# Optimization experiments

Measured on AMD Instinct MI355X. Metric: run time of the kernel, lower is better.

The kernel has to match this reference:

```python
import jax, jax.numpy as jnp
import numpy as np

B, S, E, H, D = 2, 4096, 512, 8, 64  # batch, seq, embed, heads, key_dim


def setup_inputs() -> dict:
    key = jax.random.key(0)
    ks = jax.random.split(key, 8)
    queries = jax.random.normal(ks[0], (B, S, E), dtype=jnp.float32)
    keys = jax.random.normal(ks[1], (B, S, E), dtype=jnp.float32)
    values = jax.random.normal(ks[2], (B, S, E), dtype=jnp.float32)
    mask = jax.random.randint(ks[3], (B, H, S, S), 0, 2).astype(bool)
    scale = 1.0 / np.sqrt(E)
    Wq = jax.random.normal(ks[4], (E, H * D), dtype=jnp.float32) * scale
    Wk = jax.random.normal(ks[5], (E, H * D), dtype=jnp.float32) * scale
    Wv = jax.random.normal(ks[6], (E, H * D), dtype=jnp.float32) * scale
    Wo = jax.random.normal(ks[7], (H * D, E), dtype=jnp.float32) * scale
    return {"queries": queries, "keys": keys, "values": values, "mask": mask,
            "Wq": Wq, "Wk": Wk, "Wv": Wv, "Wo": Wo}


def reference(queries, keys, values, mask, Wq, Wk, Wv, Wo):
    # QKV projections (no bias), reshape to heads: (B, S, H, D)
    q = (queries @ Wq).reshape(B, -1, H, D)
    k = (keys @ Wk).reshape(B, -1, H, D)
    v = (values @ Wv).reshape(B, -1, H, D)
    # scores: (B, H, Sq, Sk)
    scores = jnp.einsum("bqhd,bkhd->bhqk", q, k) / jnp.sqrt(jnp.float32(D))
    scores = jnp.where(mask, jnp.float32(-1e10), scores)
    attn = jax.nn.softmax(scores, axis=-1)
    out = jnp.einsum("bhqk,bkhd->bqhd", attn, v).reshape(B, -1, H * D)
    return out @ Wo
```

## Files before the change

kernel.cpp:

```cpp
#include <hip/hip_runtime.h>
#include <hip/hip_bf16.h>

#define NB 2
#define NS 4096
#define NE 512
#define NH 8
#define ND 64
#define NHD 512

typedef __attribute__((ext_vector_type(8))) short short8;
typedef __attribute__((ext_vector_type(4))) float floatx4;
typedef __attribute__((ext_vector_type(16))) float f32x16;

#define MFMA16(a, b, c) __builtin_amdgcn_mfma_f32_16x16x32_bf16((a), (b), (c), 0, 0, 0)
#define MFMA32(a, b, c) __builtin_amdgcn_mfma_f32_32x32x16_bf16((a), (b), (c), 0, 0, 0)

union Cvt8 { uint4 u; short8 s; };
static __device__ __forceinline__ short8 ld8(const __hip_bfloat16* p) {
  Cvt8 c; c.u = *(const uint4*)p; return c.s;
}
union BH { __hip_bfloat16 h; short s; };
static __device__ __forceinline__ short f2bs(float x) {
  BH u; u.h = __float2bfloat16(x); return u.s;
}
static __device__ __forceinline__ unsigned pk2(float a, float b) {
  unsigned d;
  asm("v_cvt_pk_bf16_f32 %0, %1, %2" : "=v"(d) : "v"(a), "v"(b));
  return d;
}

__global__ __launch_bounds__(256) void mask_pack(const int* __restrict__ mask,
                                                 unsigned long long* __restrict__ bits) {
  const int lane = threadIdx.x & 63;
  const long wid = (long)((blockIdx.x * 256 + threadIdx.x) >> 6);
  const long base = wid * 512;
  const int* p = mask + base * 64 + lane;
  for (int i = 0; i < 512; i += 4) {
    const int m0 = p[(long)(i + 0) * 64];
    const int m1 = p[(long)(i + 1) * 64];
    const int m2 = p[(long)(i + 2) * 64];
    const int m3 = p[(long)(i + 3) * 64];
    const unsigned long long b0 = __ballot(m0 != 0);
    const unsigned long long b1 = __ballot(m1 != 0);
    const unsigned long long b2 = __ballot(m2 != 0);
    const unsigned long long b3 = __ballot(m3 != 0);
    if (lane == 0) {
      *(ulonglong2*)(bits + base + i) = ulonglong2{b0, b1};
      *(ulonglong2*)(bits + base + i + 2) = ulonglong2{b2, b3};
    }
  }
}

__global__ __launch_bounds__(256) void wconv(
    const float* w0, const float* w1, const float* w2, const float* w3,
    __hip_bfloat16* t0, __hip_bfloat16* t1,
    __hip_bfloat16* t2, __hip_bfloat16* t3) {
  __shared__ __hip_bfloat16 tile[64][72];
  const float* src;
  __hip_bfloat16* dst;
  switch (blockIdx.z) {
    case 0: src = w0; dst = t0; break;
    case 1: src = w1; dst = t1; break;
    case 2: src = w2; dst = t2; break;
    default: src = w3; dst = t3; break;
  }
  const int tx = threadIdx.x & 63, ty = threadIdx.x >> 6;
  const int n0 = blockIdx.x * 64, k0 = blockIdx.y * 64;
  for (int r = ty; r < 64; r += 4)
    tile[r][tx] = __float2bfloat16(src[(long)(k0 + r) * 512 + n0 + tx]);
  __syncthreads();
  for (int r = ty; r < 64; r += 4)
    dst[(long)(n0 + r) * 512 + k0 + tx] = tile[tx][r];
}

__global__ __launch_bounds__(256) void gemm_qkv(
    const float* A0, const float* A1, const float* A2,
    const __hip_bfloat16* W0, const __hip_bfloat16* W1, const __hip_bfloat16* W2,
    __hip_bfloat16* O0, __hip_bfloat16* O1, __hip_bfloat16* O2) {
  const float* A;
  const __hip_bfloat16* Wt;
  __hip_bfloat16* O;
  switch (blockIdx.z) {
    case 0: A = A0; Wt = W0; O = O0; break;
    case 1: A = A1; Wt = W1; O = O1; break;
    default: A = A2; Wt = W2; O = O2; break;
  }
  const int lane = threadIdx.x & 63;
  const int w = threadIdx.x >> 6;
  const int c = lane & 15, g = lane >> 4;
  const int m0 = blockIdx.x * 64 + w * 16;
  const int n0 = blockIdx.y * 64;

  floatx4 acc[4] = {};
  const float* ap = A + (long)(m0 + c) * 512 + g * 8;
  const __hip_bfloat16* wp = Wt + (long)(n0 + c) * 512 + g * 8;
  for (int ks = 0; ks < 512; ks += 32) {
    const float4 f0 = *(const float4*)(ap + ks);
    const float4 f1 = *(const float4*)(ap + ks + 4);
    short8 a;
    a[0] = f2bs(f0.x); a[1] = f2bs(f0.y); a[2] = f2bs(f0.z); a[3] = f2bs(f0.w);
    a[4] = f2bs(f1.x); a[5] = f2bs(f1.y); a[6] = f2bs(f1.z); a[7] = f2bs(f1.w);
#pragma unroll
    for (int t = 0; t < 4; ++t) {
      short8 b = ld8(wp + t * 16 * 512 + ks);
      acc[t] = MFMA16(a, b, acc[t]);
    }
  }
  const float sc = (blockIdx.z == 0) ? 0.125f : 1.0f;
#pragma unroll
  for (int t = 0; t < 4; ++t) {
#pragma unroll
    for (int r = 0; r < 4; ++r) {
      const int m = m0 + g * 4 + r;
      const int n = n0 + t * 16 + c;
      const int bb = m >> 12, s = m & 4095, h = n >> 6, d = n & 63;
      O[(((long)bb * NH + h) * NS + s) * ND + d] = __float2bfloat16(acc[t][r] * sc);
    }
  }
}

#define VPAD 72
__device__ __forceinline__ int vswz(int row) { return ((row >> 3) & 7) * 8; }

__global__ __launch_bounds__(256) void flash_attn(
    const __hip_bfloat16* Q, const __hip_bfloat16* K, const __hip_bfloat16* V,
    const unsigned long long* __restrict__ Mb, __hip_bfloat16* AO) {
  __shared__ __hip_bfloat16 Ks[64 * VPAD];
  __shared__ __hip_bfloat16 Vt[64 * VPAD];

  const int tid = threadIdx.x;
  const int lane = tid & 63, w = tid >> 6;
  const int ql = lane & 31, hl = lane >> 5;
  const int bz = blockIdx.z, hy = blockIdx.y;
  const int q0 = blockIdx.x * 128 + w * 32;
  const long headbase = ((long)bz * NH + hy) * NS;

  short8 qf[4];
#pragma unroll
  for (int ds = 0; ds < 4; ++ds)
    qf[ds] = ld8(Q + (headbase + q0 + ql) * ND + ds * 16 + hl * 8);

  f32x16 oacc0 = {}, oacc1 = {};
  float m_i = -1e30f, l_i = 0.f;
  const unsigned long long* mrp = Mb + ((headbase + q0 + ql) << 6);

  for (int kt = 0; kt < 64; ++kt) {
    const int k0 = kt * 64;
#pragma unroll
    for (int it = 0; it < 2; ++it) {
      const int chunk = tid + it * 256;
      const int kc = chunk >> 3;
      const int dd = (chunk & 7) * 8;
      const long gbase = (headbase + k0 + kc) * ND + dd;
      *(uint4*)&Ks[kc * VPAD + dd] = *(const uint4*)(K + gbase);
      uint4 vv = *(const uint4*)(V + gbase);
      const __hip_bfloat16* ve = (const __hip_bfloat16*)&vv;
#pragma unroll
      for (int j = 0; j < 8; ++j) {
        const int row = dd + j;
        Vt[row * VPAD + (kc ^ vswz(row))] = ve[j];
      }
    }
    const unsigned long long mword = mrp[kt];
    __syncthreads();

    f32x16 s0 = {}, s1 = {};
#pragma unroll
    for (int ds = 0; ds < 4; ++ds) {
      short8 a0 = ld8(&Ks[ql * VPAD + ds * 16 + hl * 8]);
      s0 = MFMA32(a0, qf[ds], s0);
      short8 a1 = ld8(&Ks[(32 + ql) * VPAD + ds * 16 + hl * 8]);
      s1 = MFMA32(a1, qf[ds], s1);
    }

    const unsigned long long wsh = mword >> (hl * 4);
    const unsigned mlo = (unsigned)wsh;
    const unsigned mhi = (unsigned)(wsh >> 32);
    float mt = -1e30f;
#pragma unroll
    for (int r = 0; r < 16; ++r) {
      const int idx = (r & 3) + 8 * (r >> 2);
      const float a0 = ((mlo >> idx) & 1u) ? -1e10f : s0[r];
      const float a1 = ((mhi >> idx) & 1u) ? -1e10f : s1[r];
      s0[r] = a0; s1[r] = a1;
      mt = fmaxf(mt, fmaxf(a0, a1));
    }
    mt = fmaxf(mt, __shfl_xor(mt, 32));

    if (__ballot(mt > m_i + 8.0f) != 0ull) {
      const float mn = fmaxf(m_i, mt);
      const float al = __expf(m_i - mn);
      m_i = mn;
      l_i *= al;
#pragma unroll
      for (int r = 0; r < 16; ++r) {
        const float ab = __shfl(al, (r & 3) + 8 * (r >> 2) + 4 * hl);
        oacc0[r] *= ab;
        oacc1[r] *= ab;
      }
    }

    float ss = 0.f;
#pragma unroll
    for (int r = 0; r < 16; ++r) {
      const float p0 = __expf(s0[r] - m_i);
      const float p1 = __expf(s1[r] - m_i);
      s0[r] = p0; s1[r] = p1;
      ss += p0 + p1;
    }
    ss += __shfl_xor(ss, 32);
    l_i += ss;

#pragma unroll
    for (int ks = 0; ks < 4; ++ks) {
      float pp[8];
#pragma unroll
      for (int j = 0; j < 8; ++j)
        pp[j] = (ks < 2) ? ((ks & 1) ? s0[8 + j] : s0[j])
                         : ((ks & 1) ? s1[8 + j] : s1[j]);
      const unsigned pk01 = pk2(pp[0], pp[1]);
      const unsigned pk23 = pk2(pp[2], pp[3]);
      const unsigned pk45 = pk2(pp[4], pp[5]);
      const unsigned pk67 = pk2(pp[6], pp[7]);
      const unsigned send1 = hl ? pk01 : pk45;
      const unsigned send2 = hl ? pk23 : pk67;
      const unsigned recv1 = __shfl_xor(send1, 32);
      const unsigned recv2 = __shfl_xor(send2, 32);
      Cvt8 pc;
      pc.u = make_uint4(hl ? recv1 : pk01,
                        hl ? recv2 : pk23,
                        hl ? pk45 : recv1,
                        hl ? pk67 : recv2);
      const int cb = ks * 16 + hl * 8;
      const short8 v0 = ld8(&Vt[ql * VPAD + (cb ^ vswz(ql))]);
      oacc0 = MFMA32(pc.s, v0, oacc0);
      const short8 v1 = ld8(&Vt[(32 + ql) * VPAD + (cb ^ vswz(32 + ql))]);
      oacc1 = MFMA32(pc.s, v1, oacc1);
    }
    __syncthreads();
  }

#pragma unroll
  for (int r = 0; r < 16; ++r) {
    const int cr = (r & 3) + 8 * (r >> 2) + 4 * hl;
    const float lb = __shfl(l_i, cr);
    const float inv = 1.0f / lb;
    const long obase = ((long)bz * NS + q0 + cr) * NHD + hy * 64;
    AO[obase + ql] = __float2bfloat16(oacc0[r] * inv);
    AO[obase + 32 + ql] = __float2bfloat16(oacc1[r] * inv);
  }
}

__global__ __launch_bounds__(256) void gemm_out(
    const __hip_bfloat16* A, const __hip_bfloat16* Wt, float* O) {
  const int lane = threadIdx.x & 63;
  const int w = threadIdx.x >> 6;
  const int c = lane & 15, g = lane >> 4;
  const int m0 = blockIdx.x * 64 + w * 16;
  const int n0 = blockIdx.y * 64;

  floatx4 acc[4] = {};
  const __hip_bfloat16* ap = A + (long)(m0 + c) * 512 + g * 8;
  const __hip_bfloat16* wp = Wt + (long)(n0 + c) * 512 + g * 8;
  for (int ks = 0; ks < 512; ks += 32) {
    short8 a = ld8(ap + ks);
#pragma unroll
    for (int t = 0; t < 4; ++t) {
      short8 b = ld8(wp + t * 16 * 512 + ks);
      acc[t] = MFMA16(a, b, acc[t]);
    }
  }
#pragma unroll
  for (int t = 0; t < 4; ++t)
#pragma unroll
    for (int r = 0; r < 4; ++r)
      O[(long)(m0 + g * 4 + r) * 512 + n0 + t * 16 + c] = acc[t][r];
}

extern "C" void kernel_launch(void* const* d_in, const int* in_sizes, int n_in,
                              void* d_out, int out_size, void* d_ws, size_t ws_size,
                              hipStream_t stream) {
  const float* q_in = (const float*)d_in[0];
  const float* k_in = (const float*)d_in[1];
  const float* v_in = (const float*)d_in[2];
  const int* mask = (const int*)d_in[3];
  const float* Wq = (const float*)d_in[4];
  const float* Wk = (const float*)d_in[5];
  const float* Wv = (const float*)d_in[6];
  const float* Wo = (const float*)d_in[7];
  float* out = (float*)d_out;

  char* base = (char*)d_ws;
  const size_t MB = 1u << 20;
  __hip_bfloat16* wtq = (__hip_bfloat16*)(base);
  __hip_bfloat16* wtk = (__hip_bfloat16*)(base + 512 * 1024);
  __hip_bfloat16* wtv = (__hip_bfloat16*)(base + 1 * MB);
  __hip_bfloat16* wto = (__hip_bfloat16*)(base + 1 * MB + 512 * 1024);
  __hip_bfloat16* qp = (__hip_bfloat16*)(base + 2 * MB);
  __hip_bfloat16* kp = (__hip_bfloat16*)(base + 10 * MB);
  __hip_bfloat16* vp = (__hip_bfloat16*)(base + 18 * MB);
  __hip_bfloat16* ao = (__hip_bfloat16*)(base + 26 * MB);
  unsigned long long* mb = (unsigned long long*)(base + 34 * MB);

  mask_pack<<<dim3(2048), 256, 0, stream>>>(mask, mb);
  wconv<<<dim3(8, 8, 4), 256, 0, stream>>>(Wq, Wk, Wv, Wo, wtq, wtk, wtv, wto);
  gemm_qkv<<<dim3(128, 8, 3), 256, 0, stream>>>(
      q_in, k_in, v_in, wtq, wtk, wtv, qp, kp, vp);
  flash_attn<<<dim3(NS / 128, NH, NB), 256, 0, stream>>>(qp, kp, vp, mb, ao);
  gemm_out<<<dim3(128, 8), 256, 0, stream>>>(ao, wto, out);
}
```

Before: 1.752 ms.

## Fuse mask reading into flash attention and switch softmax to exp2

Removes the separate mask_pack kernel. The attention kernel now reads the int32 mask directly as int4 vectors, issuing the loads at the top of each key tile so they overlap the K/V staging. This drops one full pass over the 512MB mask plus the bitmask write/read, but each attention block now streams the raw mask itself, with per-lane row-strided accesses. It also folds log2(e) into the Q scale and uses the hardware v_exp_f32 (exp2) directly instead of __expf.

```diff
diff --git a/kernel.cpp b/kernel.cpp
--- a/kernel.cpp
+++ b/kernel.cpp
@@ -28,27 +28,10 @@
   asm("v_cvt_pk_bf16_f32 %0, %1, %2" : "=v"(d) : "v"(a), "v"(b));
   return d;
 }
-
-__global__ __launch_bounds__(256) void mask_pack(const int* __restrict__ mask,
-                                                 unsigned long long* __restrict__ bits) {
-  const int lane = threadIdx.x & 63;
-  const long wid = (long)((blockIdx.x * 256 + threadIdx.x) >> 6);
-  const long base = wid * 512;
-  const int* p = mask + base * 64 + lane;
-  for (int i = 0; i < 512; i += 4) {
-    const int m0 = p[(long)(i + 0) * 64];
-    const int m1 = p[(long)(i + 1) * 64];
-    const int m2 = p[(long)(i + 2) * 64];
-    const int m3 = p[(long)(i + 3) * 64];
-    const unsigned long long b0 = __ballot(m0 != 0);
-    const unsigned long long b1 = __ballot(m1 != 0);
-    const unsigned long long b2 = __ballot(m2 != 0);
-    const unsigned long long b3 = __ballot(m3 != 0);
-    if (lane == 0) {
-      *(ulonglong2*)(bits + base + i) = ulonglong2{b0, b1};
-      *(ulonglong2*)(bits + base + i + 2) = ulonglong2{b2, b3};
-    }
-  }
+static __device__ __forceinline__ float fexp2(float x) {
+  float r;
+  asm("v_exp_f32 %0, %1" : "=v"(r) : "v"(x));
+  return r;
 }
 
 __global__ __launch_bounds__(256) void wconv(
@@ -106,7 +89,7 @@
       acc[t] = MFMA16(a, b, acc[t]);
     }
   }
-  const float sc = (blockIdx.z == 0) ? 0.125f : 1.0f;
+  const float sc = (blockIdx.z == 0) ? 0.125f * 1.44269504f : 1.0f;
 #pragma unroll
   for (int t = 0; t < 4; ++t) {
 #pragma unroll
@@ -124,7 +107,7 @@
 
 __global__ __launch_bounds__(256) void flash_attn(
     const __hip_bfloat16* Q, const __hip_bfloat16* K, const __hip_bfloat16* V,
-    const unsigned long long* __restrict__ Mb, __hip_bfloat16* AO) {
+    const int* __restrict__ mask, __hip_bfloat16* AO) {
   __shared__ __hip_bfloat16 Ks[64 * VPAD];
   __shared__ __hip_bfloat16 Vt[64 * VPAD];
 
@@ -142,10 +125,24 @@
 
   f32x16 oacc0 = {}, oacc1 = {};
   float m_i = -1e30f, l_i = 0.f;
-  const unsigned long long* mrp = Mb + ((headbase + q0 + ql) << 6);
+  const int* mrow = mask + (headbase + q0 + ql) * (long)NS;
 
   for (int kt = 0; kt < 64; ++kt) {
     const int k0 = kt * 64;
+
+    int4 mk0, mk1, mk2, mk3, mk4, mk5, mk6, mk7;
+    {
+      const int* mp = mrow + k0 + 4 * hl;
+      mk0 = *(const int4*)(mp + 0);
+      mk1 = *(const int4*)(mp + 8);
+      mk2 = *(const int4*)(mp + 16);
+      mk3 = *(const int4*)(mp + 24);
+      mk4 = *(const int4*)(mp + 32);
+      mk5 = *(const int4*)(mp + 40);
+      mk6 = *(const int4*)(mp + 48);
+      mk7 = *(const int4*)(mp + 56);
+    }
+
 #pragma unroll
     for (int it = 0; it < 2; ++it) {
       const int chunk = tid + it * 256;
@@ -161,7 +158,6 @@
         Vt[row * VPAD + (kc ^ vswz(row))] = ve[j];
       }
     }
-    const unsigned long long mword = mrp[kt];
     __syncthreads();
 
     f32x16 s0 = {}, s1 = {};
@@ -173,23 +169,34 @@
       s1 = MFMA32(a1, qf[ds], s1);
     }
 
-    const unsigned long long wsh = mword >> (hl * 4);
-    const unsigned mlo = (unsigned)wsh;
-    const unsigned mhi = (unsigned)(wsh >> 32);
+#pragma unroll
+    for (int rr = 0; rr < 4; ++rr) {
+      int4 a, b;
+      switch (rr) {
+        case 0: a = mk0; b = mk4; break;
+        case 1: a = mk1; b = mk5; break;
+        case 2: a = mk2; b = mk6; break;
+        default: a = mk3; b = mk7; break;
+      }
+      if (a.x != 0) s0[4 * rr + 0] = -1e10f;
+      if (a.y != 0) s0[4 * rr + 1] = -1e10f;
+      if (a.z != 0) s0[4 * rr + 2] = -1e10f;
+      if (a.w != 0) s0[4 * rr + 3] = -1e10f;
+      if (b.x != 0) s1[4 * rr + 0] = -1e10f;
+      if (b.y != 0) s1[4 * rr + 1] = -1e10f;
+      if (b.z != 0) s1[4 * rr + 2] = -1e10f;
+      if (b.w != 0) s1[4 * rr + 3] = -1e10f;
+    }
+
     float mt = -1e30f;
 #pragma unroll
-    for (int r = 0; r < 16; ++r) {
-      const int idx = (r & 3) + 8 * (r >> 2);
-      const float a0 = ((mlo >> idx) & 1u) ? -1e10f : s0[r];
-      const float a1 = ((mhi >> idx) & 1u) ? -1e10f : s1[r];
-      s0[r] = a0; s1[r] = a1;
-      mt = fmaxf(mt, fmaxf(a0, a1));
-    }
+    for (int r = 0; r < 16; ++r)
+      mt = fmaxf(mt, fmaxf(s0[r], s1[r]));
     mt = fmaxf(mt, __shfl_xor(mt, 32));
 
     if (__ballot(mt > m_i + 8.0f) != 0ull) {
       const float mn = fmaxf(m_i, mt);
-      const float al = __expf(m_i - mn);
+      const float al = fexp2(m_i - mn);
       m_i = mn;
       l_i *= al;
 #pragma unroll
@@ -203,8 +210,8 @@
     float ss = 0.f;
 #pragma unroll
     for (int r = 0; r < 16; ++r) {
-      const float p0 = __expf(s0[r] - m_i);
-      const float p1 = __expf(s1[r] - m_i);
+      const float p0 = fexp2(s0[r] - m_i);
+      const float p1 = fexp2(s1[r] - m_i);
       s0[r] = p0; s1[r] = p1;
       ss += p0 + p1;
     }
@@ -300,12 +307,10 @@
   __hip_bfloat16* kp = (__hip_bfloat16*)(base + 10 * MB);
   __hip_bfloat16* vp = (__hip_bfloat16*)(base + 18 * MB);
   __hip_bfloat16* ao = (__hip_bfloat16*)(base + 26 * MB);
-  unsigned long long* mb = (unsigned long long*)(base + 34 * MB);
-
-  mask_pack<<<dim3(2048), 256, 0, stream>>>(mask, mb);
+
   wconv<<<dim3(8, 8, 4), 256, 0, stream>>>(Wq, Wk, Wv, Wo, wtq, wtk, wtv, wto);
   gemm_qkv<<<dim3(128, 8, 3), 256, 0, stream>>>(
       q_in, k_in, v_in, wtq, wtk, wtv, qp, kp, vp);
-  flash_attn<<<dim3(NS / 128, NH, NB), 256, 0, stream>>>(qp, kp, vp, mb, ao);
+  flash_attn<<<dim3(NS / 128, NH, NB), 256, 0, stream>>>(qp, kp, vp, mask, ao);
   gemm_out<<<dim3(128, 8), 256, 0, stream>>>(ao, wto, out);
 }
```

Result: faster. 1.610 ms (median of 2 runs) (-8.1%).
